# Optimization experiments

Hardware: AMD Instinct MI355X
Metric: run time of the kernel (lower is better)

The kernel has to match this reference:

```python
import jax, jax.numpy as jnp
import numpy as np

N, E, D_IN, HID, D_OUT, HEADS = 4096, 262144, 256, 256, 128, 4


def gcn_conv(x, edge_index, edge_weight, W, b):
    # PyG GCNConv: linear -> gcn_norm (add self loops, sym norm) -> scatter-add -> +bias
    n = x.shape[0]
    row, col = edge_index[0], edge_index[1]
    loop = jnp.arange(n)
    row_f = jnp.concatenate([row, loop])
    col_f = jnp.concatenate([col, loop])
    ew_f = jnp.concatenate([edge_weight, jnp.ones((n,), edge_weight.dtype)])
    deg = jax.ops.segment_sum(ew_f, col_f, num_segments=n)
    dinv = jnp.where(deg > 0, jax.lax.rsqrt(deg), 0.0)
    norm = dinv[row_f] * ew_f * dinv[col_f]  # [E+N]
    h = x @ W                                # [N, out]
    out = jax.ops.segment_sum(norm[:, None] * h[row_f], col_f, num_segments=n)
    return out + b


def mha(x, in_proj_w, in_proj_b, out_proj_w, out_proj_b):
    # torch.nn.MultiheadAttention, unbatched input [L, Emb], q=k=v=x
    L, Emb = x.shape
    dh = Emb // HEADS
    qkv = x @ in_proj_w.T + in_proj_b
    q, k, v = jnp.split(qkv, 3, axis=-1)
    rs = lambda t: t.reshape(L, HEADS, dh).transpose(1, 0, 2)  # [H, L, dh]
    q, k, v = rs(q), rs(k), rs(v)
    scores = jnp.einsum('hld,hmd->hlm', q, k) / np.float32(np.sqrt(dh))
    attn = jax.nn.softmax(scores, axis=-1)
    o = jnp.einsum('hlm,hmd->hld', attn, v).transpose(1, 0, 2).reshape(L, Emb)
    return o @ out_proj_w.T + out_proj_b


def setup_inputs() -> dict:
    key = jax.random.key(0)
    ks = jax.random.split(key, 12)
    s = 0.02
    return {
        'node_features': jax.random.normal(ks[0], (N, D_IN), jnp.float32),
        'edge_index': jax.random.randint(ks[1], (2, E), 0, N),
        'edge_weight': jax.random.uniform(ks[2], (E,), jnp.float32),
        'W1': jax.random.normal(ks[3], (D_IN, HID), jnp.float32) * s,
        'b1': jnp.zeros((HID,), jnp.float32),
        'W2': jax.random.normal(ks[4], (HID, HID), jnp.float32) * s,
        'b2': jnp.zeros((HID,), jnp.float32),
        'W3': jax.random.normal(ks[5], (HID, D_OUT), jnp.float32) * s,
        'b3': jnp.zeros((D_OUT,), jnp.float32),
        'in_proj_w': jax.random.normal(ks[6], (3 * HID, HID), jnp.float32) * s,
        'in_proj_b': jnp.zeros((3 * HID,), jnp.float32),
        'out_proj_w': jax.random.normal(ks[7], (HID, HID), jnp.float32) * s,
        'out_proj_b': jnp.zeros((HID,), jnp.float32),
    }


def reference(node_features, edge_index, edge_weight, W1, b1, W2, b2, W3, b3,
              in_proj_w, in_proj_b, out_proj_w, out_proj_b):
    ew = edge_weight.astype(jnp.float32)
    x = gcn_conv(node_features, edge_index, ew, W1, b1)
    x = jax.nn.relu(mha(x, in_proj_w, in_proj_b, out_proj_w, out_proj_b))
    # dropout is identity at inference
    x = gcn_conv(x, edge_index, ew, W2, b2)
    x = jax.nn.relu(mha(x, in_proj_w, in_proj_b, out_proj_w, out_proj_b))
    x = gcn_conv(x, edge_index, ew, W3, b3)
    return jax.nn.sigmoid(x)
```

## Files before the change

### kernel.cpp

```cpp
#include <hip/hip_runtime.h>
#include <math.h>

#define N_NODES 4096
#define N_EDGES 262144

typedef __attribute__((ext_vector_type(4))) float f32x4;
typedef __attribute__((ext_vector_type(8))) short s16x8;
typedef __attribute__((ext_vector_type(4))) unsigned short u16x4;

__device__ inline unsigned short f2bf(float f) {
    unsigned u = __builtin_bit_cast(unsigned, f);
    u += 0x7FFF + ((u >> 16) & 1);
    return (unsigned short)(u >> 16);
}
__device__ inline float bf2f(unsigned short u) {
    unsigned x = ((unsigned)u) << 16;
    return __builtin_bit_cast(float, x);
}

#define SWZ(row, colb) (((row) << 7) + ((colb) ^ (((row) & 7) << 4)))

__global__ void prep_all(const float* __restrict__ x0, const float* __restrict__ ipw,
                         const float* __restrict__ opw, const float* __restrict__ ipb,
                         const float* __restrict__ W1, const float* __restrict__ W2,
                         const float* __restrict__ W3,
                         unsigned short* __restrict__ x0b, unsigned short* __restrict__ ipwb,
                         unsigned short* __restrict__ opwb, float* __restrict__ ipbs,
                         unsigned short* __restrict__ W1t, unsigned short* __restrict__ W2t,
                         unsigned short* __restrict__ W3t,
                         float* __restrict__ deg, int* __restrict__ cnt) {
    const int NA = 262144;
    const int NB = 49152;
    const int NC = 16384;
    const int ND1 = 65536, ND2 = 65536, ND3 = 32768;
    const int NE = 768, NF = 4096;
    const int total = NA + NB + NC + ND1 + ND2 + ND3 + NE + NF;
    for (int idx = blockIdx.x * blockDim.x + threadIdx.x; idx < total;
         idx += gridDim.x * blockDim.x) {
        int t = idx;
        if (t < NA) {
            int i = t * 4;
            f32x4 v = *(const f32x4*)(x0 + i);
            u16x4 o;
#pragma unroll
            for (int j = 0; j < 4; j++) o[j] = f2bf(v[j]);
            *(u16x4*)(x0b + i) = o;
            continue;
        }
        t -= NA;
        if (t < NB) {
            int i = t * 4;
            int r = i >> 8;
            float sc = (r >= 256 && r < 512) ? 0.1803369f : 1.0f;
            f32x4 v = *(const f32x4*)(ipw + i);
            u16x4 o;
#pragma unroll
            for (int j = 0; j < 4; j++) o[j] = f2bf(v[j] * sc);
            *(u16x4*)(ipwb + i) = o;
            continue;
        }
        t -= NB;
        if (t < NC) {
            int i = t * 4;
            f32x4 v = *(const f32x4*)(opw + i);
            u16x4 o;
#pragma unroll
            for (int j = 0; j < 4; j++) o[j] = f2bf(v[j]);
            *(u16x4*)(opwb + i) = o;
            continue;
        }
        t -= NC;
        if (t < ND1) {
            int r = t & 255, c = t >> 8;
            W1t[c * 256 + r] = f2bf(W1[r * 256 + c]);
            continue;
        }
        t -= ND1;
        if (t < ND2) {
            int r = t & 255, c = t >> 8;
            W2t[c * 256 + r] = f2bf(W2[r * 256 + c]);
            continue;
        }
        t -= ND2;
        if (t < ND3) {
            int r = t & 255, c = t >> 8;
            W3t[c * 256 + r] = f2bf(W3[r * 128 + c]);
            continue;
        }
        t -= ND3;
        if (t < NE) {
            float sc = (t >= 256 && t < 512) ? 0.1803369f : 1.0f;
            ipbs[t] = ipb[t] * sc;
            continue;
        }
        t -= NE;
        deg[t] = 1.0f;
        cnt[t] = 0;
    }
}

__global__ void deg_accum(const int* __restrict__ col, const float* __restrict__ ew,
                          float* deg, int* cnt) {
    for (int e = blockIdx.x * blockDim.x + threadIdx.x; e < N_EDGES;
         e += gridDim.x * blockDim.x) {
        int c = col[e];
        atomicAdd(&deg[c], ew[e]);
        atomicAdd(&cnt[c], 1);
    }
}

__global__ __launch_bounds__(1024) void scan_offsets(const int* __restrict__ cnt,
                                                     float* __restrict__ deg,
                                                     int* off, int* fill) {
    __shared__ int s[1024];
    int tid = threadIdx.x;
#pragma unroll
    for (int q = 0; q < 4; q++) {
        int i = tid * 4 + q;
        float d = deg[i];
        deg[i] = d > 0.f ? rsqrtf(d) : 0.f;
    }
    int c0 = cnt[tid * 4 + 0], c1 = cnt[tid * 4 + 1];
    int c2 = cnt[tid * 4 + 2], c3 = cnt[tid * 4 + 3];
    int lsum = c0 + c1 + c2 + c3;
    s[tid] = lsum;
    __syncthreads();
    for (int d = 1; d < 1024; d <<= 1) {
        int v = (tid >= d) ? s[tid - d] : 0;
        __syncthreads();
        s[tid] += v;
        __syncthreads();
    }
    int incl = s[tid];
    int base = incl - lsum;
    int o0 = base, o1 = base + c0, o2 = base + c0 + c1, o3 = base + c0 + c1 + c2;
    off[tid * 4 + 0] = o0;  fill[tid * 4 + 0] = o0;
    off[tid * 4 + 1] = o1;  fill[tid * 4 + 1] = o1;
    off[tid * 4 + 2] = o2;  fill[tid * 4 + 2] = o2;
    off[tid * 4 + 3] = o3;  fill[tid * 4 + 3] = o3;
    if (tid == 1023) off[4096] = incl;
}

__global__ void scatter_edges(const int* __restrict__ row, const int* __restrict__ col,
                              const float* __restrict__ ew, const float* __restrict__ dinv,
                              int* fill, int* srow, float* snorm) {
    for (int e = blockIdx.x * blockDim.x + threadIdx.x; e < N_EDGES;
         e += gridDim.x * blockDim.x) {
        int r = row[e], c = col[e];
        int p = atomicAdd(&fill[c], 1);
        srow[p] = r;
        snorm[p] = dinv[r] * ew[e] * dinv[c];
    }
}

template <bool BIAS, int ACT, bool QKV>
__global__ __launch_bounds__(64) void gemm_bf16(const unsigned short* __restrict__ A,
                                                const unsigned short* __restrict__ B,
                                                const float* __restrict__ bias,
                                                unsigned short* __restrict__ C,
                                                unsigned short* __restrict__ Vt, int P) {
    int lane = threadIdx.x & 63;
    int lx = lane & 15, g = lane >> 4;
    int brow = blockIdx.y * 32, bcol = blockIdx.x * 64;
    const unsigned short* Ap0 = A + (size_t)(brow + lx) * 256 + g * 8;
    const unsigned short* Ap1 = Ap0 + 16 * 256;
    const unsigned short* Bp = B + (size_t)(bcol + lx) * 256 + g * 8;
    f32x4 acc[2][4];
#pragma unroll
    for (int mi = 0; mi < 2; mi++)
#pragma unroll
        for (int nt = 0; nt < 4; nt++) acc[mi][nt] = f32x4{0.f, 0.f, 0.f, 0.f};
#pragma unroll
    for (int kc = 0; kc < 8; kc++) {
        s16x8 a0 = *(const s16x8*)(Ap0 + kc * 32);
        s16x8 a1 = *(const s16x8*)(Ap1 + kc * 32);
#pragma unroll
        for (int nt = 0; nt < 4; nt++) {
            s16x8 b = *(const s16x8*)(Bp + (size_t)nt * 16 * 256 + kc * 32);
            acc[0][nt] = __builtin_amdgcn_mfma_f32_16x16x32_bf16(a0, b, acc[0][nt], 0, 0, 0);
            acc[1][nt] = __builtin_amdgcn_mfma_f32_16x16x32_bf16(a1, b, acc[1][nt], 0, 0, 0);
        }
    }
    bool isV = QKV && (bcol >= 512);
    if (!isV) {
#pragma unroll
        for (int mi = 0; mi < 2; mi++)
#pragma unroll
            for (int nt = 0; nt < 4; nt++)
#pragma unroll
                for (int r = 0; r < 4; r++) {
                    int row = brow + mi * 16 + g * 4 + r, col = bcol + nt * 16 + lx;
                    float v = acc[mi][nt][r];
                    if (BIAS) v += bias[col];
                    if (ACT == 1) v = fmaxf(v, 0.f);
                    C[(size_t)row * P + col] = f2bf(v);
                }
    } else {
        int head = (bcol - 512) >> 6;
#pragma unroll
        for (int mi = 0; mi < 2; mi++)
#pragma unroll
            for (int nt = 0; nt < 4; nt++) {
                int col = bcol + nt * 16 + lx;
                u16x4 vv;
#pragma unroll
                for (int r = 0; r < 4; r++) {
                    float v = acc[mi][nt][r];
                    if (BIAS) v += bias[col];
                    vv[r] = f2bf(v);
                }
                *(u16x4*)(Vt + (size_t)(head * 64 + nt * 16 + lx) * 4096 +
                          brow + mi * 16 + g * 4) = vv;
            }
    }
}

template <int P, bool SIG>
__global__ __launch_bounds__(64) void gcn_agg(const unsigned short* __restrict__ H,
                                              const int* __restrict__ off,
                                              const int* __restrict__ srow,
                                              const float* __restrict__ snorm,
                                              const float* __restrict__ dinv,
                                              const float* __restrict__ bias,
                                              unsigned short* __restrict__ outb,
                                              float* __restrict__ outf) {
    constexpr int CPT = P / 64;
    __shared__ int sr[64];
    __shared__ float sw[64];
    int i = blockIdx.x, tid = threadIdx.x;
    float di = dinv[i];
    float d2 = di * di;
    float acc[CPT];
    if (CPT == 4) {
        u16x4 h = *(const u16x4*)(H + (size_t)i * P + tid * 4);
#pragma unroll
        for (int j = 0; j < 4; j++) acc[j] = d2 * bf2f(h[j]);
    } else {
        unsigned h = *(const unsigned*)(H + (size_t)i * P + tid * 2);
        acc[0] = d2 * bf2f((unsigned short)(h & 0xFFFF));
        acc[1] = d2 * bf2f((unsigned short)(h >> 16));
    }
    int beg = off[i], end = off[i + 1];
    for (int base = beg; base < end; base += 64) {
        int n = min(64, end - base);
        __syncthreads();
        if (tid < n) { sr[tid] = srow[base + tid]; sw[tid] = snorm[base + tid]; }
        __syncthreads();
#pragma unroll 4
        for (int j = 0; j < n; j++) {
            float w = sw[j];
            size_t rb = (size_t)sr[j] * P;
            if (CPT == 4) {
                u16x4 h = *(const u16x4*)(H + rb + tid * 4);
#pragma unroll
                for (int q = 0; q < 4; q++) acc[q] += w * bf2f(h[q]);
            } else {
                unsigned h = *(const unsigned*)(H + rb + tid * 2);
                acc[0] += w * bf2f((unsigned short)(h & 0xFFFF));
                acc[1] += w * bf2f((unsigned short)(h >> 16));
            }
        }
    }
#pragma unroll
    for (int j = 0; j < CPT; j++) {
        int c = tid * CPT + j;
        float v = acc[j] + bias[c];
        if (SIG) {
            v = 1.f / (1.f + exp2f(-v * 1.442695f));
            outf[(size_t)i * P + c] = v;
        } else {
            outb[(size_t)i * P + c] = f2bf(v);
        }
    }
}

__global__ __launch_bounds__(256) void attn_mfma(const unsigned short* __restrict__ qkv,
                                                 const unsigned short* __restrict__ Vt,
                                                 unsigned short* __restrict__ Po,
                                                 float* __restrict__ Pl) {
    __shared__ unsigned short Ks[2][64 * 64];
    __shared__ unsigned short Vs[2][64 * 64];
    __shared__ unsigned short Ps[4][16 * 64];

    int tid = threadIdx.x;
    int wid = tid >> 6, lane = tid & 63, g = lane >> 4, lx = lane & 15;
    int head = blockIdx.y, chunk = blockIdx.z;
    int qw = blockIdx.x * 64 + wid * 16;

    s16x8 qa[2];
#pragma unroll
    for (int kc = 0; kc < 2; kc++)
        qa[kc] = *(const s16x8*)(qkv + (size_t)(qw + lx) * 768 + head * 64 + kc * 32 + g * 8);

    const unsigned short* Kg = qkv + 256 + head * 64;
    const unsigned short* VtH = Vt + (size_t)head * 64 * 4096;

    int kr0 = tid >> 3, dc0 = tid & 7;
    int kr1 = kr0 + 32;
    s16x8 stK[2], stV[2];
    auto issue = [&](int kt) {
        stK[0] = *(const s16x8*)(Kg + (size_t)(kt * 64 + kr0) * 768 + dc0 * 8);
        stK[1] = *(const s16x8*)(Kg + (size_t)(kt * 64 + kr1) * 768 + dc0 * 8);
        stV[0] = *(const s16x8*)(VtH + (size_t)kr0 * 4096 + kt * 64 + dc0 * 8);
        stV[1] = *(const s16x8*)(VtH + (size_t)kr1 * 4096 + kt * 64 + dc0 * 8);
    };
    auto commit = [&](int b) {
        *(s16x8*)((char*)Ks[b] + SWZ(kr0, dc0 * 16)) = stK[0];
        *(s16x8*)((char*)Ks[b] + SWZ(kr1, dc0 * 16)) = stK[1];
        *(s16x8*)((char*)Vs[b] + SWZ(kr0, dc0 * 16)) = stV[0];
        *(s16x8*)((char*)Vs[b] + SWZ(kr1, dc0 * 16)) = stV[1];
    };

    float lreg[4] = {0.f, 0.f, 0.f, 0.f};
    f32x4 o[4];
#pragma unroll
    for (int dt = 0; dt < 4; dt++) o[dt] = f32x4{0.f, 0.f, 0.f, 0.f};

    char* PsW = (char*)Ps[wid];

    int kt_beg = chunk * 8, kt_end = kt_beg + 8;
    issue(kt_beg);
    commit(0);
    __syncthreads();

    for (int kt = kt_beg; kt < kt_end; kt++) {
        int cur = (kt - kt_beg) & 1;
        if (kt + 1 < kt_end) issue(kt + 1);

        f32x4 s4[4];
        __builtin_amdgcn_s_setprio(1);
#pragma unroll
        for (int nt = 0; nt < 4; nt++) {
            f32x4 acc = f32x4{0.f, 0.f, 0.f, 0.f};
#pragma unroll
            for (int kc = 0; kc < 2; kc++) {
                s16x8 kb = *(const s16x8*)((char*)Ks[cur] + SWZ(nt * 16 + lx, kc * 64 + g * 16));
                acc = __builtin_amdgcn_mfma_f32_16x16x32_bf16(qa[kc], kb, acc, 0, 0, 0);
            }
            s4[nt] = acc;
        }
        __builtin_amdgcn_s_setprio(0);

#pragma unroll
        for (int nt = 0; nt < 4; nt++)
#pragma unroll
            for (int r = 0; r < 4; r++) {
                float p = exp2f(fminf(s4[nt][r], 60.f));
                lreg[r] += p;
                *(unsigned short*)(PsW + SWZ(4 * g + r, (nt * 16 + lx) * 2)) = f2bf(p);
            }

        __builtin_amdgcn_s_setprio(1);
#pragma unroll
        for (int kc = 0; kc < 2; kc++) {
            s16x8 pa = *(const s16x8*)(PsW + SWZ(lx, kc * 64 + g * 16));
#pragma unroll
            for (int dt = 0; dt < 4; dt++) {
                s16x8 vb = *(const s16x8*)((char*)Vs[cur] + SWZ(dt * 16 + lx, kc * 64 + g * 16));
                o[dt] = __builtin_amdgcn_mfma_f32_16x16x32_bf16(pa, vb, o[dt], 0, 0, 0);
            }
        }
        __builtin_amdgcn_s_setprio(0);

        if (kt + 1 < kt_end) commit(1 - cur);
        __syncthreads();
    }

#pragma unroll
    for (int r = 0; r < 4; r++) {
        float ls = lreg[r];
        ls += __shfl_xor(ls, 1, 16);
        ls += __shfl_xor(ls, 2, 16);
        ls += __shfl_xor(ls, 4, 16);
        ls += __shfl_xor(ls, 8, 16);
        int qrow = qw + 4 * g + r;
        size_t base = (size_t)(chunk * 4 + head) * 4096 + qrow;
        if (lx == 0) Pl[base] = ls;
#pragma unroll
        for (int dt = 0; dt < 4; dt++)
            Po[base * 64 + dt * 16 + lx] = f2bf(o[dt][r]);
    }
}

__global__ __launch_bounds__(256) void attn_combine(const unsigned short* __restrict__ Po,
                                                    const float* __restrict__ Pl,
                                                    unsigned short* __restrict__ att) {
    int q = blockIdx.x;
    int head = threadIdx.x >> 6, d = threadIdx.x & 63;
    float L = 0.f, ov = 0.f;
#pragma unroll
    for (int c = 0; c < 8; c++) {
        size_t base = (size_t)(c * 4 + head) * 4096 + q;
        L += Pl[base];
        ov += bf2f(Po[base * 64 + d]);
    }
    att[(size_t)q * 256 + head * 64 + d] = f2bf(ov / L);
}

extern "C" void kernel_launch(void* const* d_in, const int* in_sizes, int n_in,
                              void* d_out, int out_size, void* d_ws, size_t ws_size,
                              hipStream_t stream) {
    const float* x0  = (const float*)d_in[0];
    const int*   eix = (const int*)d_in[1];
    const float* ew  = (const float*)d_in[2];
    const float* W1  = (const float*)d_in[3];
    const float* b1  = (const float*)d_in[4];
    const float* W2  = (const float*)d_in[5];
    const float* b2  = (const float*)d_in[6];
    const float* W3  = (const float*)d_in[7];
    const float* b3  = (const float*)d_in[8];
    const float* ipw = (const float*)d_in[9];
    const float* ipb = (const float*)d_in[10];
    const float* opw = (const float*)d_in[11];
    const float* opb = (const float*)d_in[12];
    float* out = (float*)d_out;

    char* ws = (char*)d_ws;
    size_t o = 0;
    auto alloc = [&](size_t bytes) -> void* {
        void* p = ws + o;
        o = (o + bytes + 255) & ~size_t(255);
        return p;
    };
    float* dinv  = (float*)alloc(N_NODES * 4);
    int*   cnt   = (int*)alloc(N_NODES * 4);
    int*   off   = (int*)alloc((N_NODES + 1) * 4);
    int*   fill  = (int*)alloc(N_NODES * 4);
    int*   srow  = (int*)alloc(N_EDGES * 4);
    float* snorm = (float*)alloc(N_EDGES * 4);
    unsigned short* x0b  = (unsigned short*)alloc((size_t)N_NODES * 256 * 2);
    unsigned short* W1t  = (unsigned short*)alloc(256 * 256 * 2);
    unsigned short* W2t  = (unsigned short*)alloc(256 * 256 * 2);
    unsigned short* W3t  = (unsigned short*)alloc(128 * 256 * 2);
    unsigned short* ipwb = (unsigned short*)alloc(768 * 256 * 2);
    unsigned short* opwb = (unsigned short*)alloc(256 * 256 * 2);
    float* ipbs          = (float*)alloc(768 * 4);
    unsigned short* Hb   = (unsigned short*)alloc((size_t)N_NODES * 256 * 2);
    unsigned short* XAb  = (unsigned short*)alloc((size_t)N_NODES * 256 * 2);
    unsigned short* XBb  = (unsigned short*)alloc((size_t)N_NODES * 256 * 2);
    unsigned short* QKVb = (unsigned short*)alloc((size_t)N_NODES * 768 * 2);
    unsigned short* Vt   = (unsigned short*)alloc((size_t)4 * 64 * 4096 * 2);
    unsigned short* Po   = (unsigned short*)alloc((size_t)32 * 4096 * 64 * 2);
    float* Pl            = (float*)alloc((size_t)32 * 4096 * 4);

    const int* row = eix;
    const int* col = eix + N_EDGES;

    prep_all<<<1024, 256, 0, stream>>>(x0, ipw, opw, ipb, W1, W2, W3,
                                       x0b, ipwb, opwb, ipbs, W1t, W2t, W3t, dinv, cnt);
    deg_accum<<<512, 256, 0, stream>>>(col, ew, dinv, cnt);
    scan_offsets<<<1, 1024, 0, stream>>>(cnt, dinv, off, fill);
    scatter_edges<<<512, 256, 0, stream>>>(row, col, ew, dinv, fill, srow, snorm);

    gemm_bf16<false, 0, false><<<dim3(4, 128), 64, 0, stream>>>(x0b, W1t, nullptr, Hb, nullptr, 256);
    gcn_agg<256, false><<<N_NODES, 64, 0, stream>>>(Hb, off, srow, snorm, dinv, b1, XAb, nullptr);
    gemm_bf16<true, 0, true><<<dim3(12, 128), 64, 0, stream>>>(XAb, ipwb, ipbs, QKVb, Vt, 768);
    attn_mfma<<<dim3(64, 4, 8), 256, 0, stream>>>(QKVb, Vt, Po, Pl);
    attn_combine<<<N_NODES, 256, 0, stream>>>(Po, Pl, Hb);
    gemm_bf16<true, 1, false><<<dim3(4, 128), 64, 0, stream>>>(Hb, opwb, opb, XBb, nullptr, 256);
    gemm_bf16<false, 0, false><<<dim3(4, 128), 64, 0, stream>>>(XBb, W2t, nullptr, Hb, nullptr, 256);
    gcn_agg<256, false><<<N_NODES, 64, 0, stream>>>(Hb, off, srow, snorm, dinv, b2, XAb, nullptr);
    gemm_bf16<true, 0, true><<<dim3(12, 128), 64, 0, stream>>>(XAb, ipwb, ipbs, QKVb, Vt, 768);
    attn_mfma<<<dim3(64, 4, 8), 256, 0, stream>>>(QKVb, Vt, Po, Pl);
    attn_combine<<<N_NODES, 256, 0, stream>>>(Po, Pl, Hb);
    gemm_bf16<true, 1, false><<<dim3(4, 128), 64, 0, stream>>>(Hb, opwb, opb, XBb, nullptr, 256);
    gemm_bf16<false, 0, false><<<dim3(2, 128), 64, 0, stream>>>(XBb, W3t, nullptr, Hb, nullptr, 128);
    gcn_agg<128, true><<<N_NODES, 64, 0, stream>>>(Hb, off, srow, snorm, dinv, b3, nullptr, out);
}
```

Before: 309.7 us.

## Pack edge row and weight, halve attention key splits, vectorize combine

Edge rows and normalized weights are packed into one 64-bit array, so the aggregation loads one value per edge instead of two. Attention now splits keys into 4 chunks of 16 tiles instead of 8 chunks of 8, which halves the partial buffers and the combine work. Combine is vectorized so each thread handles 4 outputs. Smaller changes: degree init moves to memsets with the self-loop folded into the rsqrt, P is converted to bf16 by truncation, and K/V addressing is done with incremented pointers. Fewer attention blocks may reduce parallelism, and truncation slightly lowers accuracy.

```diff
diff --git a/kernel.cpp b/kernel.cpp
--- a/kernel.cpp
+++ b/kernel.cpp
@@ -12,6 +12,9 @@
     unsigned u = __builtin_bit_cast(unsigned, f);
     u += 0x7FFF + ((u >> 16) & 1);
     return (unsigned short)(u >> 16);
+}
+__device__ inline unsigned short f2bf_t(float f) {
+    return (unsigned short)(__builtin_bit_cast(unsigned, f) >> 16);
 }
 __device__ inline float bf2f(unsigned short u) {
     unsigned x = ((unsigned)u) << 16;
@@ -27,14 +30,13 @@
                          unsigned short* __restrict__ x0b, unsigned short* __restrict__ ipwb,
                          unsigned short* __restrict__ opwb, float* __restrict__ ipbs,
                          unsigned short* __restrict__ W1t, unsigned short* __restrict__ W2t,
-                         unsigned short* __restrict__ W3t,
-                         float* __restrict__ deg, int* __restrict__ cnt) {
+                         unsigned short* __restrict__ W3t) {
     const int NA = 262144;
     const int NB = 49152;
     const int NC = 16384;
     const int ND1 = 65536, ND2 = 65536, ND3 = 32768;
-    const int NE = 768, NF = 4096;
-    const int total = NA + NB + NC + ND1 + ND2 + ND3 + NE + NF;
+    const int NE = 768;
+    const int total = NA + NB + NC + ND1 + ND2 + ND3 + NE;
     for (int idx = blockIdx.x * blockDim.x + threadIdx.x; idx < total;
          idx += gridDim.x * blockDim.x) {
         int t = idx;
@@ -88,14 +90,10 @@
             continue;
         }
         t -= ND3;
-        if (t < NE) {
+        {
             float sc = (t >= 256 && t < 512) ? 0.1803369f : 1.0f;
             ipbs[t] = ipb[t] * sc;
-            continue;
-        }
-        t -= NE;
-        deg[t] = 1.0f;
-        cnt[t] = 0;
+        }
     }
 }
 
@@ -117,8 +115,7 @@
 #pragma unroll
     for (int q = 0; q < 4; q++) {
         int i = tid * 4 + q;
-        float d = deg[i];
-        deg[i] = d > 0.f ? rsqrtf(d) : 0.f;
+        deg[i] = rsqrtf(deg[i] + 1.0f);
     }
     int c0 = cnt[tid * 4 + 0], c1 = cnt[tid * 4 + 1];
     int c2 = cnt[tid * 4 + 2], c3 = cnt[tid * 4 + 3];
@@ -143,13 +140,15 @@
 
 __global__ void scatter_edges(const int* __restrict__ row, const int* __restrict__ col,
                               const float* __restrict__ ew, const float* __restrict__ dinv,
-                              int* fill, int* srow, float* snorm) {
+                              int* fill, unsigned long long* __restrict__ ep) {
     for (int e = blockIdx.x * blockDim.x + threadIdx.x; e < N_EDGES;
          e += gridDim.x * blockDim.x) {
         int r = row[e], c = col[e];
         int p = atomicAdd(&fill[c], 1);
-        srow[p] = r;
-        snorm[p] = dinv[r] * ew[e] * dinv[c];
+        float w = dinv[r] * ew[e] * dinv[c];
+        unsigned long long v =
+            ((unsigned long long)__builtin_bit_cast(unsigned, w) << 32) | (unsigned)r;
+        ep[p] = v;
     }
 }
 
@@ -218,15 +217,13 @@
 template <int P, bool SIG>
 __global__ __launch_bounds__(64) void gcn_agg(const unsigned short* __restrict__ H,
                                               const int* __restrict__ off,
-                                              const int* __restrict__ srow,
-                                              const float* __restrict__ snorm,
+                                              const unsigned long long* __restrict__ ep,
                                               const float* __restrict__ dinv,
                                               const float* __restrict__ bias,
                                               unsigned short* __restrict__ outb,
                                               float* __restrict__ outf) {
     constexpr int CPT = P / 64;
-    __shared__ int sr[64];
-    __shared__ float sw[64];
+    __shared__ unsigned long long se[64];
     int i = blockIdx.x, tid = threadIdx.x;
     float di = dinv[i];
     float d2 = di * di;
@@ -244,12 +241,14 @@
     for (int base = beg; base < end; base += 64) {
         int n = min(64, end - base);
         __syncthreads();
-        if (tid < n) { sr[tid] = srow[base + tid]; sw[tid] = snorm[base + tid]; }
+        if (tid < n) se[tid] = ep[base + tid];
         __syncthreads();
 #pragma unroll 4
         for (int j = 0; j < n; j++) {
-            float w = sw[j];
-            size_t rb = (size_t)sr[j] * P;
+            unsigned long long v = se[j];
+            int r = (int)(unsigned)v;
+            float w = __builtin_bit_cast(float, (unsigned)(v >> 32));
+            size_t rb = (size_t)r * P;
             if (CPT == 4) {
                 u16x4 h = *(const u16x4*)(H + rb + tid * 4);
 #pragma unroll
@@ -292,17 +291,25 @@
     for (int kc = 0; kc < 2; kc++)
         qa[kc] = *(const s16x8*)(qkv + (size_t)(qw + lx) * 768 + head * 64 + kc * 32 + g * 8);
 
-    const unsigned short* Kg = qkv + 256 + head * 64;
-    const unsigned short* VtH = Vt + (size_t)head * 64 * 4096;
-
     int kr0 = tid >> 3, dc0 = tid & 7;
     int kr1 = kr0 + 32;
+    int kt_beg = chunk * 16, kt_end = kt_beg + 16;
+
+    const unsigned short* kp0 =
+        qkv + 256 + head * 64 + (size_t)(kt_beg * 64 + kr0) * 768 + dc0 * 8;
+    const unsigned short* kp1 = kp0 + (size_t)32 * 768;
+    const unsigned short* vp0 =
+        Vt + (size_t)head * 64 * 4096 + (size_t)kr0 * 4096 + kt_beg * 64 + dc0 * 8;
+    const unsigned short* vp1 = vp0 + (size_t)32 * 4096;
+
     s16x8 stK[2], stV[2];
-    auto issue = [&](int kt) {
-        stK[0] = *(const s16x8*)(Kg + (size_t)(kt * 64 + kr0) * 768 + dc0 * 8);
-        stK[1] = *(const s16x8*)(Kg + (size_t)(kt * 64 + kr1) * 768 + dc0 * 8);
-        stV[0] = *(const s16x8*)(VtH + (size_t)kr0 * 4096 + kt * 64 + dc0 * 8);
-        stV[1] = *(const s16x8*)(VtH + (size_t)kr1 * 4096 + kt * 64 + dc0 * 8);
+    auto issue = [&]() {
+        stK[0] = *(const s16x8*)kp0;
+        stK[1] = *(const s16x8*)kp1;
+        stV[0] = *(const s16x8*)vp0;
+        stV[1] = *(const s16x8*)vp1;
+        kp0 += 64 * 768; kp1 += 64 * 768;
+        vp0 += 64; vp1 += 64;
     };
     auto commit = [&](int b) {
         *(s16x8*)((char*)Ks[b] + SWZ(kr0, dc0 * 16)) = stK[0];
@@ -318,14 +325,13 @@
 
     char* PsW = (char*)Ps[wid];
 
-    int kt_beg = chunk * 8, kt_end = kt_beg + 8;
-    issue(kt_beg);
+    issue();
     commit(0);
     __syncthreads();
 
     for (int kt = kt_beg; kt < kt_end; kt++) {
         int cur = (kt - kt_beg) & 1;
-        if (kt + 1 < kt_end) issue(kt + 1);
+        if (kt + 1 < kt_end) issue();
 
         f32x4 s4[4];
         __builtin_amdgcn_s_setprio(1);
@@ -347,7 +353,7 @@
             for (int r = 0; r < 4; r++) {
                 float p = exp2f(fminf(s4[nt][r], 60.f));
                 lreg[r] += p;
-                *(unsigned short*)(PsW + SWZ(4 * g + r, (nt * 16 + lx) * 2)) = f2bf(p);
+                *(unsigned short*)(PsW + SWZ(4 * g + r, (nt * 16 + lx) * 2)) = f2bf_t(p);
             }
 
         __builtin_amdgcn_s_setprio(1);
@@ -385,16 +391,25 @@
 __global__ __launch_bounds__(256) void attn_combine(const unsigned short* __restrict__ Po,
                                                     const float* __restrict__ Pl,
                                                     unsigned short* __restrict__ att) {
-    int q = blockIdx.x;
-    int head = threadIdx.x >> 6, d = threadIdx.x & 63;
-    float L = 0.f, ov = 0.f;
-#pragma unroll
-    for (int c = 0; c < 8; c++) {
+    int tid = threadIdx.x;
+    int q = blockIdx.x * 4 + (tid >> 6);
+    int lane = tid & 63;
+    int head = lane >> 4, quad = lane & 15;
+    float L = 0.f;
+    f32x4 ov = {0.f, 0.f, 0.f, 0.f};
+#pragma unroll
+    for (int c = 0; c < 4; c++) {
         size_t base = (size_t)(c * 4 + head) * 4096 + q;
         L += Pl[base];
-        ov += bf2f(Po[base * 64 + d]);
-    }
-    att[(size_t)q * 256 + head * 64 + d] = f2bf(ov / L);
+        u16x4 p = *(const u16x4*)(Po + base * 64 + quad * 4);
+#pragma unroll
+        for (int k = 0; k < 4; k++) ov[k] += bf2f(p[k]);
+    }
+    float inv = 1.0f / L;
+    u16x4 r;
+#pragma unroll
+    for (int k = 0; k < 4; k++) r[k] = f2bf(ov[k] * inv);
+    *(u16x4*)(att + (size_t)q * 256 + head * 64 + quad * 4) = r;
 }
 
 extern "C" void kernel_launch(void* const* d_in, const int* in_sizes, int n_in,
@@ -426,8 +441,7 @@
     int*   cnt   = (int*)alloc(N_NODES * 4);
     int*   off   = (int*)alloc((N_NODES + 1) * 4);
     int*   fill  = (int*)alloc(N_NODES * 4);
-    int*   srow  = (int*)alloc(N_EDGES * 4);
-    float* snorm = (float*)alloc(N_EDGES * 4);
+    unsigned long long* ep = (unsigned long long*)alloc((size_t)N_EDGES * 8);
     unsigned short* x0b  = (unsigned short*)alloc((size_t)N_NODES * 256 * 2);
     unsigned short* W1t  = (unsigned short*)alloc(256 * 256 * 2);
     unsigned short* W2t  = (unsigned short*)alloc(256 * 256 * 2);
@@ -440,30 +454,32 @@
     unsigned short* XBb  = (unsigned short*)alloc((size_t)N_NODES * 256 * 2);
     unsigned short* QKVb = (unsigned short*)alloc((size_t)N_NODES * 768 * 2);
     unsigned short* Vt   = (unsigned short*)alloc((size_t)4 * 64 * 4096 * 2);
-    unsigned short* Po   = (unsigned short*)alloc((size_t)32 * 4096 * 64 * 2);
-    float* Pl            = (float*)alloc((size_t)32 * 4096 * 4);
+    unsigned short* Po   = (unsigned short*)alloc((size_t)16 * 4096 * 64 * 2);
+    float* Pl            = (float*)alloc((size_t)16 * 4096 * 4);
 
     const int* row = eix;
     const int* col = eix + N_EDGES;
 
-    prep_all<<<1024, 256, 0, stream>>>(x0, ipw, opw, ipb, W1, W2, W3,
-                                       x0b, ipwb, opwb, ipbs, W1t, W2t, W3t, dinv, cnt);
+    hipMemsetAsync(dinv, 0, N_NODES * 4, stream);
+    hipMemsetAsync(cnt, 0, N_NODES * 4, stream);
+    prep_all<<<512, 256, 0, stream>>>(x0, ipw, opw, ipb, W1, W2, W3,
+                                      x0b, ipwb, opwb, ipbs, W1t, W2t, W3t);
     deg_accum<<<512, 256, 0, stream>>>(col, ew, dinv, cnt);
     scan_offsets<<<1, 1024, 0, stream>>>(cnt, dinv, off, fill);
-    scatter_edges<<<512, 256, 0, stream>>>(row, col, ew, dinv, fill, srow, snorm);
+    scatter_edges<<<512, 256, 0, stream>>>(row, col, ew, dinv, fill, ep);
 
     gemm_bf16<false, 0, false><<<dim3(4, 128), 64, 0, stream>>>(x0b, W1t, nullptr, Hb, nullptr, 256);
-    gcn_agg<256, false><<<N_NODES, 64, 0, stream>>>(Hb, off, srow, snorm, dinv, b1, XAb, nullptr);
+    gcn_agg<256, false><<<N_NODES, 64, 0, stream>>>(Hb, off, ep, dinv, b1, XAb, nullptr);
     gemm_bf16<true, 0, true><<<dim3(12, 128), 64, 0, stream>>>(XAb, ipwb, ipbs, QKVb, Vt, 768);
-    attn_mfma<<<dim3(64, 4, 8), 256, 0, stream>>>(QKVb, Vt, Po, Pl);
-    attn_combine<<<N_NODES, 256, 0, stream>>>(Po, Pl, Hb);
+    attn_mfma<<<dim3(64, 4, 4), 256, 0, stream>>>(QKVb, Vt, Po, Pl);
+    attn_combine<<<N_NODES / 4, 256, 0, stream>>>(Po, Pl, Hb);
     gemm_bf16<true, 1, false><<<dim3(4, 128), 64, 0, stream>>>(Hb, opwb, opb, XBb, nullptr, 256);
     gemm_bf16<false, 0, false><<<dim3(4, 128), 64, 0, stream>>>(XBb, W2t, nullptr, Hb, nullptr, 256);
-    gcn_agg<256, false><<<N_NODES, 64, 0, stream>>>(Hb, off, srow, snorm, dinv, b2, XAb, nullptr);
+    gcn_agg<256, false><<<N_NODES, 64, 0, stream>>>(Hb, off, ep, dinv, b2, XAb, nullptr);
     gemm_bf16<true, 0, true><<<dim3(12, 128), 64, 0, stream>>>(XAb, ipwb, ipbs, QKVb, Vt, 768);
-    attn_mfma<<<dim3(64, 4, 8), 256, 0, stream>>>(QKVb, Vt, Po, Pl);
-    attn_combine<<<N_NODES, 256, 0, stream>>>(Po, Pl, Hb);
+    attn_mfma<<<dim3(64, 4, 4), 256, 0, stream>>>(QKVb, Vt, Po, Pl);
+    attn_combine<<<N_NODES / 4, 256, 0, stream>>>(Po, Pl, Hb);
     gemm_bf16<true, 1, false><<<dim3(4, 128), 64, 0, stream>>>(Hb, opwb, opb, XBb, nullptr, 256);
     gemm_bf16<false, 0, false><<<dim3(2, 128), 64, 0, stream>>>(XBb, W3t, nullptr, Hb, nullptr, 128);
-    gcn_agg<128, true><<<N_NODES, 64, 0, stream>>>(Hb, off, srow, snorm, dinv, b3, nullptr, out);
-}
+    gcn_agg<128, true><<<N_NODES, 64, 0, stream>>>(Hb, off, ep, dinv, b3, nullptr, out);
+}
```

Result: no change. 303.8 us (-1.9%).
